# Performance work log

Measured on AMD Instinct MI355X. Metric: run time of the kernel, lower is better.

The kernel has to match this reference:

```python
import jax, jax.numpy as jnp
import numpy as np

B, T, D, H = 4096, 128, 32, 64

def _gru_layer(x, W_ih, W_hh, b_ih, b_hh):
    # x: [B, T, in]; W_ih: [3H, in]; W_hh: [3H, H]
    xg = jnp.einsum('bti,gi->btg', x, W_ih) + b_ih  # [B, T, 3H] input gates, one big GEMM
    def step(h, xg_t):
        gh = h @ W_hh.T + b_hh                      # [B, 3H]
        xr, xz, xn = jnp.split(xg_t, 3, axis=-1)
        hr, hz, hn = jnp.split(gh, 3, axis=-1)
        r = jax.nn.sigmoid(xr + hr)
        z = jax.nn.sigmoid(xz + hz)
        n = jnp.tanh(xn + r * hn)
        h_new = (1.0 - z) * n + z * h
        return h_new, h_new
    h0 = jnp.zeros((x.shape[0], W_hh.shape[1]), x.dtype)
    _, hs = jax.lax.scan(step, h0, jnp.swapaxes(xg, 0, 1))  # scan over time
    return jnp.swapaxes(hs, 0, 1)                   # [B, T, H]

def setup_inputs() -> dict:
    key = jax.random.key(0)
    ks = jax.random.split(key, 12)
    s = 0.1
    return {
        'x':     jax.random.normal(ks[0], (B, T, D), jnp.float32),
        'W_ih0': jax.random.normal(ks[1], (3 * H, D), jnp.float32) * s,
        'W_hh0': jax.random.normal(ks[2], (3 * H, H), jnp.float32) * s,
        'b_ih0': jax.random.normal(ks[3], (3 * H,), jnp.float32) * s,
        'b_hh0': jax.random.normal(ks[4], (3 * H,), jnp.float32) * s,
        'W_ih1': jax.random.normal(ks[5], (3 * H, H), jnp.float32) * s,
        'W_hh1': jax.random.normal(ks[6], (3 * H, H), jnp.float32) * s,
        'b_ih1': jax.random.normal(ks[7], (3 * H,), jnp.float32) * s,
        'b_hh1': jax.random.normal(ks[8], (3 * H,), jnp.float32) * s,
        'fc_w':  jax.random.normal(ks[9], (1, H), jnp.float32) * s,
        'fc_b':  jax.random.normal(ks[10], (1,), jnp.float32) * s,
    }

def reference(x, W_ih0, W_hh0, b_ih0, b_hh0, W_ih1, W_hh1, b_ih1, b_hh1, fc_w, fc_b):
    h1 = _gru_layer(x, W_ih0, W_hh0, b_ih0, b_hh0)   # layer 0
    h2 = _gru_layer(h1, W_ih1, W_hh1, b_ih1, b_hh1)  # layer 1
    last = h2[:, -1, :]                              # [B, H]
    out = last @ fc_w.T + fc_b                       # [B, 1]
    return jnp.squeeze(out, axis=-1)                 # [B]
```

## Files before the change

### kernel.cpp

```cpp
#include <hip/hip_runtime.h>

typedef _Float16 f16;
typedef f16 f16x8 __attribute__((ext_vector_type(8)));
typedef f16 f16x4 __attribute__((ext_vector_type(4)));
typedef __fp16 h16x2 __attribute__((ext_vector_type(2)));
typedef float f32x4 __attribute__((ext_vector_type(4)));
typedef float f32x2 __attribute__((ext_vector_type(2)));

#define MFMA16(A, B, C) __builtin_amdgcn_mfma_f32_16x16x32_f16((A), (B), (C), 0, 0, 0)

#define LDS_BARRIER() asm volatile("s_waitcnt lgkmcnt(0)\n\ts_barrier" ::: "memory")

__device__ __forceinline__ float E2(float x) {
#if __has_builtin(__builtin_amdgcn_exp2f)
  return __builtin_amdgcn_exp2f(x);
#else
  return __expf(x * 0.69314718056f);
#endif
}

__device__ __forceinline__ f16x8 cvt8(float4 a, float4 b) {
  union { h16x2 h[4]; f16x8 v; } u;
  u.h[0] = __builtin_amdgcn_cvt_pkrtz(a.x, a.y);
  u.h[1] = __builtin_amdgcn_cvt_pkrtz(a.z, a.w);
  u.h[2] = __builtin_amdgcn_cvt_pkrtz(b.x, b.y);
  u.h[3] = __builtin_amdgcn_cvt_pkrtz(b.z, b.w);
  return u.v;
}

__device__ __forceinline__ void gates_pair(f32x2 aR, f32x2 aZ, f32x2 aXN,
                                           f32x2 aHN, f32x2& hs) {
  const float K = -1.44269504f;
  f32x2 mR = aR * K;
  f32x2 mZ = aZ * K;
  f32x2 ea, eb;
  ea[0] = E2(mR[0]); ea[1] = E2(mR[1]);
  eb[0] = E2(mZ[0]); eb[1] = E2(mZ[1]);
  f32x2 pa = ea + 1.0f;
  f32x2 pb = eb + 1.0f;
  f32x2 prod = pa * pb;
  f32x2 inv;
  inv[0] = __builtin_amdgcn_rcpf(prod[0]);
  inv[1] = __builtin_amdgcn_rcpf(prod[1]);
  f32x2 rg = pb * inv;
  f32x2 zg = pa * inv;
  f32x2 y = rg * aHN + aXN;
  f32x2 my = y * (2.0f * K);
  f32x2 c;
  c[0] = E2(my[0]); c[1] = E2(my[1]);
  f32x2 num = 1.0f - c;
  f32x2 den = 1.0f + c;
  f32x2 rin;
  rin[0] = __builtin_amdgcn_rcpf(den[0]);
  rin[1] = __builtin_amdgcn_rcpf(den[1]);
  f32x2 ng = num * rin;
  hs = zg * (hs - ng) + ng;
}

__launch_bounds__(512, 2)
__global__ void gru_fused(const float* __restrict__ x,
                          const float* __restrict__ Wih0, const float* __restrict__ Whh0,
                          const float* __restrict__ bih0, const float* __restrict__ bhh0,
                          const float* __restrict__ Wih1, const float* __restrict__ Whh1,
                          const float* __restrict__ bih1, const float* __restrict__ bhh1,
                          const float* __restrict__ fcw, const float* __restrict__ fcb,
                          float* __restrict__ out) {
  __shared__ f16 H0[2][1024];
  __shared__ f16 H1[2][1024];
  __shared__ float red[4][16];

  const int tid = threadIdx.x;
  const int wave = tid >> 6;
  const int lane = tid & 63;
  const int l15 = lane & 15;
  const int q = lane >> 4;
  const int wa = wave & 3;
  const bool isB = wave >= 4;
  const int b0 = blockIdx.x * 16;

  for (int i = tid; i < 2048; i += 512) {
    ((f16*)H0)[i] = (f16)0.0f;
    ((f16*)H1)[i] = (f16)0.0f;
  }

  f16x8 wAx[3];
  f16x8 wAh[3][2];
  f16x8 wBx[3][2];
  f16x8 wBh[3][2];
  f32x4 bR, bZ, bXN, bHN;
  float fw[4] = {0.f, 0.f, 0.f, 0.f};

  if (!isB) {
#pragma unroll
    for (int g = 0; g < 3; ++g) {
      const int row = g * 64 + 16 * wa + l15;
      const float* p = Wih0 + row * 32 + q * 8;
      wAx[g] = cvt8(*(const float4*)p, *(const float4*)(p + 4));
#pragma unroll
      for (int kf = 0; kf < 2; ++kf) {
        const float* ph = Whh0 + row * 64 + kf * 32 + q * 8;
        wAh[g][kf] = cvt8(*(const float4*)ph, *(const float4*)(ph + 4));
      }
    }
#pragma unroll
    for (int r = 0; r < 4; ++r) {
      const int o = 16 * wa + 4 * q + r;
      bR[r] = bih0[o] + bhh0[o];
      bZ[r] = bih0[64 + o] + bhh0[64 + o];
      bXN[r] = bih0[128 + o];
      bHN[r] = bhh0[128 + o];
    }
  } else {
#pragma unroll
    for (int g = 0; g < 3; ++g) {
      const int row = g * 64 + 16 * wa + l15;
#pragma unroll
      for (int kf = 0; kf < 2; ++kf) {
        const float* p1 = Wih1 + row * 64 + kf * 32 + q * 8;
        wBx[g][kf] = cvt8(*(const float4*)p1, *(const float4*)(p1 + 4));
        const float* p2 = Whh1 + row * 64 + kf * 32 + q * 8;
        wBh[g][kf] = cvt8(*(const float4*)p2, *(const float4*)(p2 + 4));
      }
    }
#pragma unroll
    for (int r = 0; r < 4; ++r) {
      const int o = 16 * wa + 4 * q + r;
      bR[r] = bih1[o] + bhh1[o];
      bZ[r] = bih1[64 + o] + bhh1[64 + o];
      bXN[r] = bih1[128 + o];
      bHN[r] = bhh1[128 + o];
      fw[r] = fcw[o];
    }
  }
  const float fcb0 = fcb[0];

  f32x2 hs01 = {0.f, 0.f}, hs23 = {0.f, 0.f};

  const int wk0 = 16 * wa + 4 * q;
  const int widx = ((wk0 >> 3) * 16 + l15) * 8 + (wk0 & 7);

  auto stepA = [&](const f16* H0r, f16* H0w, float4 xav, float4 xbv) {
    const f16x8 xf = cvt8(xav, xbv);
    const f16x8 h0f0 = *(const f16x8*)&H0r[lane * 8];
    const f16x8 h0f1 = *(const f16x8*)&H0r[512 + lane * 8];
    f32x4 aR = bR, aZ = bZ, aXN = bXN, aHN = bHN;
    aR = MFMA16(wAx[0], xf, aR);
    aZ = MFMA16(wAx[1], xf, aZ);
    aXN = MFMA16(wAx[2], xf, aXN);
    aR = MFMA16(wAh[0][0], h0f0, aR);
    aZ = MFMA16(wAh[1][0], h0f0, aZ);
    aHN = MFMA16(wAh[2][0], h0f0, aHN);
    aR = MFMA16(wAh[0][1], h0f1, aR);
    aZ = MFMA16(wAh[1][1], h0f1, aZ);
    aHN = MFMA16(wAh[2][1], h0f1, aHN);
    gates_pair(f32x2{aR[0], aR[1]}, f32x2{aZ[0], aZ[1]},
               f32x2{aXN[0], aXN[1]}, f32x2{aHN[0], aHN[1]}, hs01);
    gates_pair(f32x2{aR[2], aR[3]}, f32x2{aZ[2], aZ[3]},
               f32x2{aXN[2], aXN[3]}, f32x2{aHN[2], aHN[3]}, hs23);
    union { h16x2 h2[2]; f16x4 v; } uw;
    uw.h2[0] = __builtin_amdgcn_cvt_pkrtz(hs01[0], hs01[1]);
    uw.h2[1] = __builtin_amdgcn_cvt_pkrtz(hs23[0], hs23[1]);
    *(f16x4*)&H0w[widx] = uw.v;
  };

  auto stepB = [&](const f16* H0r, const f16* H1r, f16* H1w) {
    const f16x8 g0 = *(const f16x8*)&H0r[lane * 8];
    const f16x8 g1 = *(const f16x8*)&H0r[512 + lane * 8];
    const f16x8 h1f0 = *(const f16x8*)&H1r[lane * 8];
    const f16x8 h1f1 = *(const f16x8*)&H1r[512 + lane * 8];
    f32x4 aR = bR, aZ = bZ, aXN = bXN, aHN = bHN;
    aR = MFMA16(wBx[0][0], g0, aR);
    aZ = MFMA16(wBx[1][0], g0, aZ);
    aXN = MFMA16(wBx[2][0], g0, aXN);
    aR = MFMA16(wBx[0][1], g1, aR);
    aZ = MFMA16(wBx[1][1], g1, aZ);
    aXN = MFMA16(wBx[2][1], g1, aXN);
    aR = MFMA16(wBh[0][0], h1f0, aR);
    aZ = MFMA16(wBh[1][0], h1f0, aZ);
    aHN = MFMA16(wBh[2][0], h1f0, aHN);
    aR = MFMA16(wBh[0][1], h1f1, aR);
    aZ = MFMA16(wBh[1][1], h1f1, aZ);
    aHN = MFMA16(wBh[2][1], h1f1, aHN);
    gates_pair(f32x2{aR[0], aR[1]}, f32x2{aZ[0], aZ[1]},
               f32x2{aXN[0], aXN[1]}, f32x2{aHN[0], aHN[1]}, hs01);
    gates_pair(f32x2{aR[2], aR[3]}, f32x2{aZ[2], aZ[3]},
               f32x2{aXN[2], aXN[3]}, f32x2{aHN[2], aHN[3]}, hs23);
    union { h16x2 h2[2]; f16x4 v; } uw;
    uw.h2[0] = __builtin_amdgcn_cvt_pkrtz(hs01[0], hs01[1]);
    uw.h2[1] = __builtin_amdgcn_cvt_pkrtz(hs23[0], hs23[1]);
    *(f16x4*)&H1w[widx] = uw.v;
  };

  __syncthreads();

  const float* xbase = x + (size_t)(b0 + l15) * 4096 + q * 8;
  float4 xa0, xb0, xa1, xb1;
  if (!isB) {
    xa0 = *(const float4*)xbase;
    xb0 = *(const float4*)(xbase + 4);
    xa1 = *(const float4*)(xbase + 32);
    xb1 = *(const float4*)(xbase + 36);
  }

  for (int t = 0; t < 128; t += 2) {
    if (!isB) {
      const float4 cxa = xa0, cxb = xb0;
      if (t + 2 < 128) {
        const float* xp = xbase + (t + 2) * 32;
        xa0 = *(const float4*)xp;
        xb0 = *(const float4*)(xp + 4);
      }
      stepA(H0[0], H0[1], cxa, cxb);
    } else if (t > 0) {
      stepB(H0[0], H1[0], H1[1]);
    }
    LDS_BARRIER();

    if (!isB) {
      const float4 cxa = xa1, cxb = xb1;
      if (t + 3 < 128) {
        const float* xp = xbase + (t + 3) * 32;
        xa1 = *(const float4*)xp;
        xb1 = *(const float4*)(xp + 4);
      }
      stepA(H0[1], H0[0], cxa, cxb);
    } else {
      stepB(H0[1], H1[1], H1[0]);
    }
    LDS_BARRIER();
  }
  if (isB) stepB(H0[0], H1[0], H1[1]);

  if (isB) {
    float partial = fw[0] * hs01[0] + fw[1] * hs01[1] + fw[2] * hs23[0] + fw[3] * hs23[1];
    partial += __shfl_down(partial, 16, 64);
    partial += __shfl_down(partial, 32, 64);
    if (lane < 16) red[wa][l15] = partial;
  }
  __syncthreads();
  if (tid < 16) out[b0 + tid] = red[0][tid] + red[1][tid] + red[2][tid] + red[3][tid] + fcb0;
}

extern "C" void kernel_launch(void* const* d_in, const int* in_sizes, int n_in,
                              void* d_out, int out_size, void* d_ws, size_t ws_size,
                              hipStream_t stream) {
  (void)in_sizes; (void)n_in; (void)out_size; (void)d_ws; (void)ws_size;
  const float* x    = (const float*)d_in[0];
  const float* Wih0 = (const float*)d_in[1];
  const float* Whh0 = (const float*)d_in[2];
  const float* bih0 = (const float*)d_in[3];
  const float* bhh0 = (const float*)d_in[4];
  const float* Wih1 = (const float*)d_in[5];
  const float* Whh1 = (const float*)d_in[6];
  const float* bih1 = (const float*)d_in[7];
  const float* bhh1 = (const float*)d_in[8];
  const float* fcw  = (const float*)d_in[9];
  const float* fcb  = (const float*)d_in[10];
  float* out = (float*)d_out;

  gru_fused<<<256, 512, 0, stream>>>(x, Wih0, Whh0, bih0, bhh0,
                                     Wih1, Whh1, bih1, bhh1, fcw, fcb, out);
}
```

Measured before the change: 177.2 us.

## Halve block to 4 waves, each wave computing two 16-row hidden tiles

Each block now runs 4 waves instead of 8, with every wave handling 32 hidden units (two 16-unit sub-tiles) per layer rather than 16. The aim is to cut per-step barrier cost and LDS fragment reload redundancy, since the shared h fragments are loaded once and reused across both sub-tiles. The trade-off is twice as many weight registers per wave and less wave-level parallelism for hiding MFMA and transcendental latency, with only 4 waves per CU across 256 blocks.

```diff
diff --git a/kernel.cpp b/kernel.cpp
--- a/kernel.cpp
+++ b/kernel.cpp
@@ -57,7 +57,7 @@
   hs = zg * (hs - ng) + ng;
 }
 
-__launch_bounds__(512, 2)
+__launch_bounds__(256, 1)
 __global__ void gru_fused(const float* __restrict__ x,
                           const float* __restrict__ Wih0, const float* __restrict__ Whh0,
                           const float* __restrict__ bih0, const float* __restrict__ bhh0,
@@ -67,100 +67,117 @@
                           float* __restrict__ out) {
   __shared__ f16 H0[2][1024];
   __shared__ f16 H1[2][1024];
-  __shared__ float red[4][16];
+  __shared__ float red[2][16];
 
   const int tid = threadIdx.x;
   const int wave = tid >> 6;
   const int lane = tid & 63;
   const int l15 = lane & 15;
   const int q = lane >> 4;
-  const int wa = wave & 3;
-  const bool isB = wave >= 4;
+  const int w = wave & 1;
+  const bool isB = wave >= 2;
   const int b0 = blockIdx.x * 16;
 
-  for (int i = tid; i < 2048; i += 512) {
+  for (int i = tid; i < 2048; i += 256) {
     ((f16*)H0)[i] = (f16)0.0f;
     ((f16*)H1)[i] = (f16)0.0f;
   }
 
-  f16x8 wAx[3];
-  f16x8 wAh[3][2];
-  f16x8 wBx[3][2];
-  f16x8 wBh[3][2];
-  f32x4 bR, bZ, bXN, bHN;
-  float fw[4] = {0.f, 0.f, 0.f, 0.f};
+  f16x8 wAx[3][2];
+  f16x8 wAh[3][2][2];
+  f16x8 wBx[3][2][2];
+  f16x8 wBh[3][2][2];
+  f32x4 bRu[2], bZu[2], bXNu[2], bHNu[2];
+  float fw[2][4] = {{0.f, 0.f, 0.f, 0.f}, {0.f, 0.f, 0.f, 0.f}};
 
   if (!isB) {
 #pragma unroll
     for (int g = 0; g < 3; ++g) {
-      const int row = g * 64 + 16 * wa + l15;
-      const float* p = Wih0 + row * 32 + q * 8;
-      wAx[g] = cvt8(*(const float4*)p, *(const float4*)(p + 4));
-#pragma unroll
-      for (int kf = 0; kf < 2; ++kf) {
-        const float* ph = Whh0 + row * 64 + kf * 32 + q * 8;
-        wAh[g][kf] = cvt8(*(const float4*)ph, *(const float4*)(ph + 4));
-      }
-    }
-#pragma unroll
-    for (int r = 0; r < 4; ++r) {
-      const int o = 16 * wa + 4 * q + r;
-      bR[r] = bih0[o] + bhh0[o];
-      bZ[r] = bih0[64 + o] + bhh0[64 + o];
-      bXN[r] = bih0[128 + o];
-      bHN[r] = bhh0[128 + o];
-    }
+#pragma unroll
+      for (int u = 0; u < 2; ++u) {
+        const int row = g * 64 + 32 * w + 16 * u + l15;
+        const float* p = Wih0 + row * 32 + q * 8;
+        wAx[g][u] = cvt8(*(const float4*)p, *(const float4*)(p + 4));
+#pragma unroll
+        for (int kf = 0; kf < 2; ++kf) {
+          const float* ph = Whh0 + row * 64 + kf * 32 + q * 8;
+          wAh[g][u][kf] = cvt8(*(const float4*)ph, *(const float4*)(ph + 4));
+        }
+      }
+    }
+#pragma unroll
+    for (int u = 0; u < 2; ++u)
+#pragma unroll
+      for (int r = 0; r < 4; ++r) {
+        const int o = 32 * w + 16 * u + 4 * q + r;
+        bRu[u][r] = bih0[o] + bhh0[o];
+        bZu[u][r] = bih0[64 + o] + bhh0[64 + o];
+        bXNu[u][r] = bih0[128 + o];
+        bHNu[u][r] = bhh0[128 + o];
+      }
   } else {
 #pragma unroll
     for (int g = 0; g < 3; ++g) {
-      const int row = g * 64 + 16 * wa + l15;
-#pragma unroll
-      for (int kf = 0; kf < 2; ++kf) {
-        const float* p1 = Wih1 + row * 64 + kf * 32 + q * 8;
-        wBx[g][kf] = cvt8(*(const float4*)p1, *(const float4*)(p1 + 4));
-        const float* p2 = Whh1 + row * 64 + kf * 32 + q * 8;
-        wBh[g][kf] = cvt8(*(const float4*)p2, *(const float4*)(p2 + 4));
-      }
-    }
-#pragma unroll
-    for (int r = 0; r < 4; ++r) {
-      const int o = 16 * wa + 4 * q + r;
-      bR[r] = bih1[o] + bhh1[o];
-      bZ[r] = bih1[64 + o] + bhh1[64 + o];
-      bXN[r] = bih1[128 + o];
-      bHN[r] = bhh1[128 + o];
-      fw[r] = fcw[o];
-    }
+#pragma unroll
+      for (int u = 0; u < 2; ++u) {
+        const int row = g * 64 + 32 * w + 16 * u + l15;
+#pragma unroll
+        for (int kf = 0; kf < 2; ++kf) {
+          const float* p1 = Wih1 + row * 64 + kf * 32 + q * 8;
+          wBx[g][u][kf] = cvt8(*(const float4*)p1, *(const float4*)(p1 + 4));
+          const float* p2 = Whh1 + row * 64 + kf * 32 + q * 8;
+          wBh[g][u][kf] = cvt8(*(const float4*)p2, *(const float4*)(p2 + 4));
+        }
+      }
+    }
+#pragma unroll
+    for (int u = 0; u < 2; ++u)
+#pragma unroll
+      for (int r = 0; r < 4; ++r) {
+        const int o = 32 * w + 16 * u + 4 * q + r;
+        bRu[u][r] = bih1[o] + bhh1[o];
+        bZu[u][r] = bih1[64 + o] + bhh1[64 + o];
+        bXNu[u][r] = bih1[128 + o];
+        bHNu[u][r] = bhh1[128 + o];
+        fw[u][r] = fcw[o];
+      }
   }
   const float fcb0 = fcb[0];
 
-  f32x2 hs01 = {0.f, 0.f}, hs23 = {0.f, 0.f};
-
-  const int wk0 = 16 * wa + 4 * q;
-  const int widx = ((wk0 >> 3) * 16 + l15) * 8 + (wk0 & 7);
+  f32x2 hs01[2] = {{0.f, 0.f}, {0.f, 0.f}};
+  f32x2 hs23[2] = {{0.f, 0.f}, {0.f, 0.f}};
+
+  int widxu[2];
+#pragma unroll
+  for (int u = 0; u < 2; ++u) {
+    const int wk0 = 32 * w + 16 * u + 4 * q;
+    widxu[u] = ((wk0 >> 3) * 16 + l15) * 8 + (wk0 & 7);
+  }
 
   auto stepA = [&](const f16* H0r, f16* H0w, float4 xav, float4 xbv) {
     const f16x8 xf = cvt8(xav, xbv);
     const f16x8 h0f0 = *(const f16x8*)&H0r[lane * 8];
     const f16x8 h0f1 = *(const f16x8*)&H0r[512 + lane * 8];
-    f32x4 aR = bR, aZ = bZ, aXN = bXN, aHN = bHN;
-    aR = MFMA16(wAx[0], xf, aR);
-    aZ = MFMA16(wAx[1], xf, aZ);
-    aXN = MFMA16(wAx[2], xf, aXN);
-    aR = MFMA16(wAh[0][0], h0f0, aR);
-    aZ = MFMA16(wAh[1][0], h0f0, aZ);
-    aHN = MFMA16(wAh[2][0], h0f0, aHN);
-    aR = MFMA16(wAh[0][1], h0f1, aR);
-    aZ = MFMA16(wAh[1][1], h0f1, aZ);
-    aHN = MFMA16(wAh[2][1], h0f1, aHN);
-    gates_pair(f32x2{aR[0], aR[1]}, f32x2{aZ[0], aZ[1]},
-               f32x2{aXN[0], aXN[1]}, f32x2{aHN[0], aHN[1]}, hs01);
-    gates_pair(f32x2{aR[2], aR[3]}, f32x2{aZ[2], aZ[3]},
-               f32x2{aXN[2], aXN[3]}, f32x2{aHN[2], aHN[3]}, hs23);
-    union { h16x2 h2[2]; f16x4 v; } uw;
-    uw.h2[0] = __builtin_amdgcn_cvt_pkrtz(hs01[0], hs01[1]);
-    uw.h2[1] = __builtin_amdgcn_cvt_pkrtz(hs23[0], hs23[1]);
-    *(f16x4*)&H0w[widx] = uw.v;
+#pragma unroll
+    for (int u = 0; u < 2; ++u) {
+      f32x4 aR = MFMA16(wAx[0][u], xf, bRu[u]);
+      f32x4 aZ = MFMA16(wAx[1][u], xf, bZu[u]);
+      f32x4 aXN = MFMA16(wAx[2][u], xf, bXNu[u]);
+      f32x4 aHN = MFMA16(wAh[2][u][0], h0f0, bHNu[u]);
+      aR = MFMA16(wAh[0][u][0], h0f0, aR);
+      aZ = MFMA16(wAh[1][u][0], h0f0, aZ);
+      aR = MFMA16(wAh[0][u][1], h0f1, aR);
+      aZ = MFMA16(wAh[1][u][1], h0f1, aZ);
+      aHN = MFMA16(wAh[2][u][1], h0f1, aHN);
+      gates_pair(f32x2{aR[0], aR[1]}, f32x2{aZ[0], aZ[1]},
+                 f32x2{aXN[0], aXN[1]}, f32x2{aHN[0], aHN[1]}, hs01[u]);
+      gates_pair(f32x2{aR[2], aR[3]}, f32x2{aZ[2], aZ[3]},
+                 f32x2{aXN[2], aXN[3]}, f32x2{aHN[2], aHN[3]}, hs23[u]);
+      union { h16x2 h2[2]; f16x4 v; } uw;
+      uw.h2[0] = __builtin_amdgcn_cvt_pkrtz(hs01[u][0], hs01[u][1]);
+      uw.h2[1] = __builtin_amdgcn_cvt_pkrtz(hs23[u][0], hs23[u][1]);
+      *(f16x4*)&H0w[widxu[u]] = uw.v;
+    }
   };
 
   auto stepB = [&](const f16* H0r, const f16* H1r, f16* H1w) {
@@ -168,27 +185,29 @@
     const f16x8 g1 = *(const f16x8*)&H0r[512 + lane * 8];
     const f16x8 h1f0 = *(const f16x8*)&H1r[lane * 8];
     const f16x8 h1f1 = *(const f16x8*)&H1r[512 + lane * 8];
-    f32x4 aR = bR, aZ = bZ, aXN = bXN, aHN = bHN;
-    aR = MFMA16(wBx[0][0], g0, aR);
-    aZ = MFMA16(wBx[1][0], g0, aZ);
-    aXN = MFMA16(wBx[2][0], g0, aXN);
-    aR = MFMA16(wBx[0][1], g1, aR);
-    aZ = MFMA16(wBx[1][1], g1, aZ);
-    aXN = MFMA16(wBx[2][1], g1, aXN);
-    aR = MFMA16(wBh[0][0], h1f0, aR);
-    aZ = MFMA16(wBh[1][0], h1f0, aZ);
-    aHN = MFMA16(wBh[2][0], h1f0, aHN);
-    aR = MFMA16(wBh[0][1], h1f1, aR);
-    aZ = MFMA16(wBh[1][1], h1f1, aZ);
-    aHN = MFMA16(wBh[2][1], h1f1, aHN);
-    gates_pair(f32x2{aR[0], aR[1]}, f32x2{aZ[0], aZ[1]},
-               f32x2{aXN[0], aXN[1]}, f32x2{aHN[0], aHN[1]}, hs01);
-    gates_pair(f32x2{aR[2], aR[3]}, f32x2{aZ[2], aZ[3]},
-               f32x2{aXN[2], aXN[3]}, f32x2{aHN[2], aHN[3]}, hs23);
-    union { h16x2 h2[2]; f16x4 v; } uw;
-    uw.h2[0] = __builtin_amdgcn_cvt_pkrtz(hs01[0], hs01[1]);
-    uw.h2[1] = __builtin_amdgcn_cvt_pkrtz(hs23[0], hs23[1]);
-    *(f16x4*)&H1w[widx] = uw.v;
+#pragma unroll
+    for (int u = 0; u < 2; ++u) {
+      f32x4 aR = MFMA16(wBx[0][u][0], g0, bRu[u]);
+      f32x4 aZ = MFMA16(wBx[1][u][0], g0, bZu[u]);
+      f32x4 aXN = MFMA16(wBx[2][u][0], g0, bXNu[u]);
+      f32x4 aHN = MFMA16(wBh[2][u][0], h1f0, bHNu[u]);
+      aR = MFMA16(wBx[0][u][1], g1, aR);
+      aZ = MFMA16(wBx[1][u][1], g1, aZ);
+      aXN = MFMA16(wBx[2][u][1], g1, aXN);
+      aHN = MFMA16(wBh[2][u][1], h1f1, aHN);
+      aR = MFMA16(wBh[0][u][0], h1f0, aR);
+      aZ = MFMA16(wBh[1][u][0], h1f0, aZ);
+      aR = MFMA16(wBh[0][u][1], h1f1, aR);
+      aZ = MFMA16(wBh[1][u][1], h1f1, aZ);
+      gates_pair(f32x2{aR[0], aR[1]}, f32x2{aZ[0], aZ[1]},
+                 f32x2{aXN[0], aXN[1]}, f32x2{aHN[0], aHN[1]}, hs01[u]);
+      gates_pair(f32x2{aR[2], aR[3]}, f32x2{aZ[2], aZ[3]},
+                 f32x2{aXN[2], aXN[3]}, f32x2{aHN[2], aHN[3]}, hs23[u]);
+      union { h16x2 h2[2]; f16x4 v; } uw;
+      uw.h2[0] = __builtin_amdgcn_cvt_pkrtz(hs01[u][0], hs01[u][1]);
+      uw.h2[1] = __builtin_amdgcn_cvt_pkrtz(hs23[u][0], hs23[u][1]);
+      *(f16x4*)&H1w[widxu[u]] = uw.v;
+    }
   };
 
   __syncthreads();
@@ -232,13 +251,17 @@
   if (isB) stepB(H0[0], H1[0], H1[1]);
 
   if (isB) {
-    float partial = fw[0] * hs01[0] + fw[1] * hs01[1] + fw[2] * hs23[0] + fw[3] * hs23[1];
+    float partial = 0.f;
+#pragma unroll
+    for (int u = 0; u < 2; ++u)
+      partial += fw[u][0] * hs01[u][0] + fw[u][1] * hs01[u][1] +
+                 fw[u][2] * hs23[u][0] + fw[u][3] * hs23[u][1];
     partial += __shfl_down(partial, 16, 64);
     partial += __shfl_down(partial, 32, 64);
-    if (lane < 16) red[wa][l15] = partial;
+    if (lane < 16) red[w][l15] = partial;
   }
   __syncthreads();
-  if (tid < 16) out[b0 + tid] = red[0][tid] + red[1][tid] + red[2][tid] + red[3][tid] + fcb0;
+  if (tid < 16) out[b0 + tid] = red[0][tid] + red[1][tid] + fcb0;
 }
 
 extern "C" void kernel_launch(void* const* d_in, const int* in_sizes, int n_in,
@@ -258,6 +281,6 @@
   const float* fcb  = (const float*)d_in[10];
   float* out = (float*)d_out;
 
-  gru_fused<<<256, 512, 0, stream>>>(x, Wih0, Whh0, bih0, bhh0,
+  gru_fused<<<256, 256, 0, stream>>>(x, Wih0, Whh0, bih0, bhh0,
                                      Wih1, Whh1, bih1, bhh1, fcw, fcb, out);
 }
```

New measurement: 203.1 us. 14.6% more time.

## Merge layer-0 and layer-1 waves so each wave computes both GRU layers

Applied to the files above, without the earlier changes.

Replaces the 8-wave block, where waves 0-3 ran layer 0 and waves 4-7 ran layer 1, with a 4-wave block in which each wave runs both layers' MFMAs and gate math in one phase. The layer-0 hidden fragments loaded from LDS are reused as layer-1 input, which removes duplicate LDS reads. Barriers now sync 4 waves instead of 8. The trade-off is higher register pressure per wave, since it holds both layers' weights, and less latency hiding because each wave does its two layers' work in sequence.

```diff
diff --git a/kernel.cpp b/kernel.cpp
--- a/kernel.cpp
+++ b/kernel.cpp
@@ -57,7 +57,7 @@
   hs = zg * (hs - ng) + ng;
 }
 
-__launch_bounds__(512, 2)
+__launch_bounds__(256, 1)
 __global__ void gru_fused(const float* __restrict__ x,
                           const float* __restrict__ Wih0, const float* __restrict__ Whh0,
                           const float* __restrict__ bih0, const float* __restrict__ bhh0,
@@ -70,15 +70,13 @@
   __shared__ float red[4][16];
 
   const int tid = threadIdx.x;
-  const int wave = tid >> 6;
+  const int w = tid >> 6;
   const int lane = tid & 63;
   const int l15 = lane & 15;
   const int q = lane >> 4;
-  const int wa = wave & 3;
-  const bool isB = wave >= 4;
   const int b0 = blockIdx.x * 16;
 
-  for (int i = tid; i < 2048; i += 512) {
+  for (int i = tid; i < 2048; i += 256) {
     ((f16*)H0)[i] = (f16)0.0f;
     ((f16*)H1)[i] = (f16)0.0f;
   }
@@ -87,155 +85,163 @@
   f16x8 wAh[3][2];
   f16x8 wBx[3][2];
   f16x8 wBh[3][2];
-  f32x4 bR, bZ, bXN, bHN;
-  float fw[4] = {0.f, 0.f, 0.f, 0.f};
-
-  if (!isB) {
 #pragma unroll
-    for (int g = 0; g < 3; ++g) {
-      const int row = g * 64 + 16 * wa + l15;
-      const float* p = Wih0 + row * 32 + q * 8;
-      wAx[g] = cvt8(*(const float4*)p, *(const float4*)(p + 4));
+  for (int g = 0; g < 3; ++g) {
+    const int row = g * 64 + 16 * w + l15;
+    const float* p = Wih0 + row * 32 + q * 8;
+    wAx[g] = cvt8(*(const float4*)p, *(const float4*)(p + 4));
 #pragma unroll
-      for (int kf = 0; kf < 2; ++kf) {
-        const float* ph = Whh0 + row * 64 + kf * 32 + q * 8;
-        wAh[g][kf] = cvt8(*(const float4*)ph, *(const float4*)(ph + 4));
-      }
-    }
+    for (int kf = 0; kf < 2; ++kf) {
+      const float* ph = Whh0 + row * 64 + kf * 32 + q * 8;
+      wAh[g][kf] = cvt8(*(const float4*)ph, *(const float4*)(ph + 4));
+      const float* p1 = Wih1 + row * 64 + kf * 32 + q * 8;
+      wBx[g][kf] = cvt8(*(const float4*)p1, *(const float4*)(p1 + 4));
+      const float* p2 = Whh1 + row * 64 + kf * 32 + q * 8;
+      wBh[g][kf] = cvt8(*(const float4*)p2, *(const float4*)(p2 + 4));
+    }
+  }
+
+  f32x4 bR0, bZ0, bXN0, bHN0, bR1, bZ1, bXN1, bHN1;
+  float fw[4];
 #pragma unroll
-    for (int r = 0; r < 4; ++r) {
-      const int o = 16 * wa + 4 * q + r;
-      bR[r] = bih0[o] + bhh0[o];
-      bZ[r] = bih0[64 + o] + bhh0[64 + o];
-      bXN[r] = bih0[128 + o];
-      bHN[r] = bhh0[128 + o];
-    }
-  } else {
-#pragma unroll
-    for (int g = 0; g < 3; ++g) {
-      const int row = g * 64 + 16 * wa + l15;
-#pragma unroll
-      for (int kf = 0; kf < 2; ++kf) {
-        const float* p1 = Wih1 + row * 64 + kf * 32 + q * 8;
-        wBx[g][kf] = cvt8(*(const float4*)p1, *(const float4*)(p1 + 4));
-        const float* p2 = Whh1 + row * 64 + kf * 32 + q * 8;
-        wBh[g][kf] = cvt8(*(const float4*)p2, *(const float4*)(p2 + 4));
-      }
-    }
-#pragma unroll
-    for (int r = 0; r < 4; ++r) {
-      const int o = 16 * wa + 4 * q + r;
-      bR[r] = bih1[o] + bhh1[o];
-      bZ[r] = bih1[64 + o] + bhh1[64 + o];
-      bXN[r] = bih1[128 + o];
-      bHN[r] = bhh1[128 + o];
-      fw[r] = fcw[o];
-    }
+  for (int r = 0; r < 4; ++r) {
+    const int o = 16 * w + 4 * q + r;
+    bR0[r] = bih0[o] + bhh0[o];
+    bZ0[r] = bih0[64 + o] + bhh0[64 + o];
+    bXN0[r] = bih0[128 + o];
+    bHN0[r] = bhh0[128 + o];
+    bR1[r] = bih1[o] + bhh1[o];
+    bZ1[r] = bih1[64 + o] + bhh1[64 + o];
+    bXN1[r] = bih1[128 + o];
+    bHN1[r] = bhh1[128 + o];
+    fw[r] = fcw[o];
   }
   const float fcb0 = fcb[0];
 
-  f32x2 hs01 = {0.f, 0.f}, hs23 = {0.f, 0.f};
-
-  const int wk0 = 16 * wa + 4 * q;
+  f32x2 h0s01 = {0.f, 0.f}, h0s23 = {0.f, 0.f};
+  f32x2 h1s01 = {0.f, 0.f}, h1s23 = {0.f, 0.f};
+
+  const int wk0 = 16 * w + 4 * q;
   const int widx = ((wk0 >> 3) * 16 + l15) * 8 + (wk0 & 7);
 
-  auto stepA = [&](const f16* H0r, f16* H0w, float4 xav, float4 xbv) {
-    const f16x8 xf = cvt8(xav, xbv);
+  auto phase = [&](const f16* H0r, f16* H0w, const f16* H1r, f16* H1w,
+                   float4 xav, float4 xbv, bool doB) {
     const f16x8 h0f0 = *(const f16x8*)&H0r[lane * 8];
     const f16x8 h0f1 = *(const f16x8*)&H0r[512 + lane * 8];
-    f32x4 aR = bR, aZ = bZ, aXN = bXN, aHN = bHN;
-    aR = MFMA16(wAx[0], xf, aR);
-    aZ = MFMA16(wAx[1], xf, aZ);
-    aXN = MFMA16(wAx[2], xf, aXN);
+    const f16x8 xf = cvt8(xav, xbv);
+    f32x4 aR = MFMA16(wAx[0], xf, bR0);
+    f32x4 aZ = MFMA16(wAx[1], xf, bZ0);
+    f32x4 aXN = MFMA16(wAx[2], xf, bXN0);
+    f32x4 aHN = MFMA16(wAh[2][0], h0f0, bHN0);
     aR = MFMA16(wAh[0][0], h0f0, aR);
     aZ = MFMA16(wAh[1][0], h0f0, aZ);
-    aHN = MFMA16(wAh[2][0], h0f0, aHN);
     aR = MFMA16(wAh[0][1], h0f1, aR);
     aZ = MFMA16(wAh[1][1], h0f1, aZ);
     aHN = MFMA16(wAh[2][1], h0f1, aHN);
-    gates_pair(f32x2{aR[0], aR[1]}, f32x2{aZ[0], aZ[1]},
-               f32x2{aXN[0], aXN[1]}, f32x2{aHN[0], aHN[1]}, hs01);
-    gates_pair(f32x2{aR[2], aR[3]}, f32x2{aZ[2], aZ[3]},
-               f32x2{aXN[2], aXN[3]}, f32x2{aHN[2], aHN[3]}, hs23);
-    union { h16x2 h2[2]; f16x4 v; } uw;
-    uw.h2[0] = __builtin_amdgcn_cvt_pkrtz(hs01[0], hs01[1]);
-    uw.h2[1] = __builtin_amdgcn_cvt_pkrtz(hs23[0], hs23[1]);
-    *(f16x4*)&H0w[widx] = uw.v;
+    if (doB) {
+      const f16x8 h1f0 = *(const f16x8*)&H1r[lane * 8];
+      const f16x8 h1f1 = *(const f16x8*)&H1r[512 + lane * 8];
+      f32x4 cR = MFMA16(wBx[0][0], h0f0, bR1);
+      f32x4 cZ = MFMA16(wBx[1][0], h0f0, bZ1);
+      f32x4 cXN = MFMA16(wBx[2][0], h0f0, bXN1);
+      f32x4 cHN = MFMA16(wBh[2][0], h1f0, bHN1);
+      cR = MFMA16(wBx[0][1], h0f1, cR);
+      cZ = MFMA16(wBx[1][1], h0f1, cZ);
+      cXN = MFMA16(wBx[2][1], h0f1, cXN);
+      cHN = MFMA16(wBh[2][1], h1f1, cHN);
+      cR = MFMA16(wBh[0][0], h1f0, cR);
+      cZ = MFMA16(wBh[1][0], h1f0, cZ);
+      cR = MFMA16(wBh[0][1], h1f1, cR);
+      cZ = MFMA16(wBh[1][1], h1f1, cZ);
+      gates_pair(f32x2{aR[0], aR[1]}, f32x2{aZ[0], aZ[1]},
+                 f32x2{aXN[0], aXN[1]}, f32x2{aHN[0], aHN[1]}, h0s01);
+      gates_pair(f32x2{aR[2], aR[3]}, f32x2{aZ[2], aZ[3]},
+                 f32x2{aXN[2], aXN[3]}, f32x2{aHN[2], aHN[3]}, h0s23);
+      union { h16x2 h2[2]; f16x4 v; } uw0;
+      uw0.h2[0] = __builtin_amdgcn_cvt_pkrtz(h0s01[0], h0s01[1]);
+      uw0.h2[1] = __builtin_amdgcn_cvt_pkrtz(h0s23[0], h0s23[1]);
+      *(f16x4*)&H0w[widx] = uw0.v;
+      gates_pair(f32x2{cR[0], cR[1]}, f32x2{cZ[0], cZ[1]},
+                 f32x2{cXN[0], cXN[1]}, f32x2{cHN[0], cHN[1]}, h1s01);
+      gates_pair(f32x2{cR[2], cR[3]}, f32x2{cZ[2], cZ[3]},
+                 f32x2{cXN[2], cXN[3]}, f32x2{cHN[2], cHN[3]}, h1s23);
+      union { h16x2 h2[2]; f16x4 v; } uw1;
+      uw1.h2[0] = __builtin_amdgcn_cvt_pkrtz(h1s01[0], h1s01[1]);
+      uw1.h2[1] = __builtin_amdgcn_cvt_pkrtz(h1s23[0], h1s23[1]);
+      *(f16x4*)&H1w[widx] = uw1.v;
+    } else {
+      gates_pair(f32x2{aR[0], aR[1]}, f32x2{aZ[0], aZ[1]},
+                 f32x2{aXN[0], aXN[1]}, f32x2{aHN[0], aHN[1]}, h0s01);
+      gates_pair(f32x2{aR[2], aR[3]}, f32x2{aZ[2], aZ[3]},
+                 f32x2{aXN[2], aXN[3]}, f32x2{aHN[2], aHN[3]}, h0s23);
+      union { h16x2 h2[2]; f16x4 v; } uw0;
+      uw0.h2[0] = __builtin_amdgcn_cvt_pkrtz(h0s01[0], h0s01[1]);
+      uw0.h2[1] = __builtin_amdgcn_cvt_pkrtz(h0s23[0], h0s23[1]);
+      *(f16x4*)&H0w[widx] = uw0.v;
+    }
   };
 
-  auto stepB = [&](const f16* H0r, const f16* H1r, f16* H1w) {
-    const f16x8 g0 = *(const f16x8*)&H0r[lane * 8];
-    const f16x8 g1 = *(const f16x8*)&H0r[512 + lane * 8];
+  auto phaseB = [&](const f16* H0r, const f16* H1r) {
+    const f16x8 h0f0 = *(const f16x8*)&H0r[lane * 8];
+    const f16x8 h0f1 = *(const f16x8*)&H0r[512 + lane * 8];
     const f16x8 h1f0 = *(const f16x8*)&H1r[lane * 8];
     const f16x8 h1f1 = *(const f16x8*)&H1r[512 + lane * 8];
-    f32x4 aR = bR, aZ = bZ, aXN = bXN, aHN = bHN;
-    aR = MFMA16(wBx[0][0], g0, aR);
-    aZ = MFMA16(wBx[1][0], g0, aZ);
-    aXN = MFMA16(wBx[2][0], g0, aXN);
-    aR = MFMA16(wBx[0][1], g1, aR);
-    aZ = MFMA16(wBx[1][1], g1, aZ);
-    aXN = MFMA16(wBx[2][1], g1, aXN);
-    aR = MFMA16(wBh[0][0], h1f0, aR);
-    aZ = MFMA16(wBh[1][0], h1f0, aZ);
-    aHN = MFMA16(wBh[2][0], h1f0, aHN);
-    aR = MFMA16(wBh[0][1], h1f1, aR);
-    aZ = MFMA16(wBh[1][1], h1f1, aZ);
-    aHN = MFMA16(wBh[2][1], h1f1, aHN);
-    gates_pair(f32x2{aR[0], aR[1]}, f32x2{aZ[0], aZ[1]},
-               f32x2{aXN[0], aXN[1]}, f32x2{aHN[0], aHN[1]}, hs01);
-    gates_pair(f32x2{aR[2], aR[3]}, f32x2{aZ[2], aZ[3]},
-               f32x2{aXN[2], aXN[3]}, f32x2{aHN[2], aHN[3]}, hs23);
-    union { h16x2 h2[2]; f16x4 v; } uw;
-    uw.h2[0] = __builtin_amdgcn_cvt_pkrtz(hs01[0], hs01[1]);
-    uw.h2[1] = __builtin_amdgcn_cvt_pkrtz(hs23[0], hs23[1]);
-    *(f16x4*)&H1w[widx] = uw.v;
+    f32x4 cR = MFMA16(wBx[0][0], h0f0, bR1);
+    f32x4 cZ = MFMA16(wBx[1][0], h0f0, bZ1);
+    f32x4 cXN = MFMA16(wBx[2][0], h0f0, bXN1);
+    f32x4 cHN = MFMA16(wBh[2][0], h1f0, bHN1);
+    cR = MFMA16(wBx[0][1], h0f1, cR);
+    cZ = MFMA16(wBx[1][1], h0f1, cZ);
+    cXN = MFMA16(wBx[2][1], h0f1, cXN);
+    cHN = MFMA16(wBh[2][1], h1f1, cHN);
+    cR = MFMA16(wBh[0][0], h1f0, cR);
+    cZ = MFMA16(wBh[1][0], h1f0, cZ);
+    cR = MFMA16(wBh[0][1], h1f1, cR);
+    cZ = MFMA16(wBh[1][1], h1f1, cZ);
+    gates_pair(f32x2{cR[0], cR[1]}, f32x2{cZ[0], cZ[1]},
+               f32x2{cXN[0], cXN[1]}, f32x2{cHN[0], cHN[1]}, h1s01);
+    gates_pair(f32x2{cR[2], cR[3]}, f32x2{cZ[2], cZ[3]},
+               f32x2{cXN[2], cXN[3]}, f32x2{cHN[2], cHN[3]}, h1s23);
   };
 
   __syncthreads();
 
   const float* xbase = x + (size_t)(b0 + l15) * 4096 + q * 8;
-  float4 xa0, xb0, xa1, xb1;
-  if (!isB) {
-    xa0 = *(const float4*)xbase;
-    xb0 = *(const float4*)(xbase + 4);
-    xa1 = *(const float4*)(xbase + 32);
-    xb1 = *(const float4*)(xbase + 36);
-  }
+  float4 xa0 = *(const float4*)xbase;
+  float4 xb0 = *(const float4*)(xbase + 4);
+  float4 xa1 = *(const float4*)(xbase + 32);
+  float4 xb1 = *(const float4*)(xbase + 36);
 
   for (int t = 0; t < 128; t += 2) {
-    if (!isB) {
+    {
       const float4 cxa = xa0, cxb = xb0;
       if (t + 2 < 128) {
         const float* xp = xbase + (t + 2) * 32;
         xa0 = *(const float4*)xp;
         xb0 = *(const float4*)(xp + 4);
       }
-      stepA(H0[0], H0[1], cxa, cxb);
-    } else if (t > 0) {
-      stepB(H0[0], H1[0], H1[1]);
+      phase(H0[0], H0[1], H1[0], H1[1], cxa, cxb, t > 0);
     }
     LDS_BARRIER();
-
-    if (!isB) {
+    {
       const float4 cxa = xa1, cxb = xb1;
       if (t + 3 < 128) {
         const float* xp = xbase + (t + 3) * 32;
         xa1 = *(const float4*)xp;
         xb1 = *(const float4*)(xp + 4);
       }
-      stepA(H0[1], H0[0], cxa, cxb);
-    } else {
-      stepB(H0[1], H1[1], H1[0]);
+      phase(H0[1], H0[0], H1[1], H1[0], cxa, cxb, true);
     }
     LDS_BARRIER();
   }
-  if (isB) stepB(H0[0], H1[0], H1[1]);
-
-  if (isB) {
-    float partial = fw[0] * hs01[0] + fw[1] * hs01[1] + fw[2] * hs23[0] + fw[3] * hs23[1];
+  phaseB(H0[0], H1[0]);
+
+  {
+    float partial = fw[0] * h1s01[0] + fw[1] * h1s01[1] +
+                    fw[2] * h1s23[0] + fw[3] * h1s23[1];
     partial += __shfl_down(partial, 16, 64);
     partial += __shfl_down(partial, 32, 64);
-    if (lane < 16) red[wa][l15] = partial;
+    if (lane < 16) red[w][l15] = partial;
   }
   __syncthreads();
   if (tid < 16) out[b0 + tid] = red[0][tid] + red[1][tid] + red[2][tid] + red[3][tid] + fcb0;
@@ -258,6 +264,6 @@
   const float* fcb  = (const float*)d_in[10];
   float* out = (float*)d_out;
 
-  gru_fused<<<256, 512, 0, stream>>>(x, Wih0, Whh0, bih0, bhh0,
+  gru_fused<<<256, 256, 0, stream>>>(x, Wih0, Whh0, bih0, bhh0,
                                      Wih1, Whh1, bih1, bhh1, fcw, fcb, out);
 }
```

Result: slower. 188.5 us (+6.4%).
